# Kernel tuning notes

Measured on AMD Instinct MI355X. Metric: run time of the kernel, lower is better.

The kernel has to match this reference:

```python
import jax, jax.numpy as jnp
import numpy as np

BLOCK = 32  # mxfp8 block size along K


def setup_inputs() -> dict:
    key = jax.random.key(0)
    ks = jax.random.split(key, 7)
    TOK, IN, OUT, RANK = 8192, 4096, 4096, 64
    return {
        "input": jax.random.normal(ks[0], (TOK, IN), dtype=jnp.float32),
        "weight_q": jax.random.normal(ks[1], (OUT, IN), dtype=jnp.float32),
        "block_scale": jax.random.uniform(ks[2], (OUT, IN // BLOCK), dtype=jnp.float32),
        "bias": jax.random.normal(ks[3], (OUT,), dtype=jnp.float32),
        "svd_u": jax.random.normal(ks[4], (OUT, RANK), dtype=jnp.float32),
        "svd_s": jax.random.uniform(ks[5], (RANK,), dtype=jnp.float32),
        "svd_v": jax.random.normal(ks[6], (IN, RANK), dtype=jnp.float32),
    }


def _dequant_mxfp8(weight_q, block_scale):
    # weight_q: [M, K], block_scale: [M, K//BLOCK] -> per-block scaled weight [M, K]
    M, K = weight_q.shape
    nb = K // BLOCK
    w = weight_q.reshape(M, nb, BLOCK) * block_scale.reshape(M, nb, 1)
    return w.reshape(M, K)


def reference(input, weight_q, block_scale, bias, svd_u, svd_s, svd_v):
    # SVD outlier branch: ((input @ V) * S) @ U^T
    outlier = ((input @ svd_v) * svd_s[None, :]) @ svd_u.T  # [TOK, OUT]
    # Dequantize mxfp8 weight then linear: input @ W^T + bias
    w = _dequant_mxfp8(weight_q, block_scale)
    residual = input @ w.T + bias[None, :]
    return outlier + residual
```

## Files before the change

### kernel.cpp

```cpp
#include <hip/hip_runtime.h>
#include <stdint.h>

typedef unsigned short ushort_t;
typedef __attribute__((ext_vector_type(8))) short short8;
typedef __attribute__((ext_vector_type(8))) unsigned short ushort8;
typedef __attribute__((ext_vector_type(4))) float f32x4;

#define TOK 8192
#define DIM_IN 4096
#define DIM_OUT 4096
#define RANK 64
#define NT (DIM_IN / 64)

__device__ __forceinline__ ushort_t f2bf(float f) {
    unsigned u = __float_as_uint(f);
    unsigned r = (u + 0x7fffu + ((u >> 16) & 1u)) >> 16;
    return (ushort_t)r;
}

__device__ __forceinline__ void gload16(const void* g, void* l) {
    __builtin_amdgcn_global_load_lds(
        (const __attribute__((address_space(1))) unsigned int*)g,
        (__attribute__((address_space(3))) unsigned int*)l,
        16, 0, 0);
}

__global__ __launch_bounds__(256) void prep_input_k(const float* __restrict__ in,
                                                    ushort_t* __restrict__ out) {
    size_t idx = (size_t)blockIdx.x * 256 + threadIdx.x;
    const float4* p = (const float4*)(in + idx * 8);
    float4 f0 = p[0], f1 = p[1];
    ushort8 o;
    o[0] = f2bf(f0.x); o[1] = f2bf(f0.y); o[2] = f2bf(f0.z); o[3] = f2bf(f0.w);
    o[4] = f2bf(f1.x); o[5] = f2bf(f1.y); o[6] = f2bf(f1.z); o[7] = f2bf(f1.w);
    *(ushort8*)(out + idx * 8) = o;
}

__global__ __launch_bounds__(256) void prep_weight_k(const float* __restrict__ wq,
                                                     const float* __restrict__ scale,
                                                     const float* __restrict__ U,
                                                     const float* __restrict__ s,
                                                     const float* __restrict__ V,
                                                     ushort_t* __restrict__ Wb) {
    __shared__ float Us[128][64];
    __shared__ float Vs[128][64];
    int tid = threadIdx.x;
    int ob = blockIdx.x >> 5;
    int kb = blockIdx.x & 31;

#pragma unroll
    for (int j = 0; j < 8; ++j) {
        int c = j * 256 + tid;
        int row = c >> 4;
        int col = (c & 15) * 4;
        float4 u = *(const float4*)&U[(size_t)(ob * 128 + row) * RANK + col];
        float4 sv = *(const float4*)&s[col];
        u.x *= sv.x; u.y *= sv.y; u.z *= sv.z; u.w *= sv.w;
        *(float4*)&Us[row][col] = u;
        float4 v = *(const float4*)&V[(size_t)(kb * 128 + row) * RANK + col];
        *(float4*)&Vs[row][col] = v;
    }
    __syncthreads();

    int ty = tid >> 4, tx = tid & 15;
    float acc[8][8];
#pragma unroll
    for (int i = 0; i < 8; ++i)
#pragma unroll
        for (int j = 0; j < 8; ++j) acc[i][j] = 0.f;

#pragma unroll 4
    for (int r4 = 0; r4 < 16; ++r4) {
        float4 u[8], v[8];
#pragma unroll
        for (int i = 0; i < 8; ++i) u[i] = *(const float4*)&Us[ty * 8 + i][r4 * 4];
#pragma unroll
        for (int j = 0; j < 8; ++j) v[j] = *(const float4*)&Vs[tx * 8 + j][r4 * 4];
#pragma unroll
        for (int i = 0; i < 8; ++i)
#pragma unroll
            for (int j = 0; j < 8; ++j)
                acc[i][j] += u[i].x * v[j].x + u[i].y * v[j].y + u[i].z * v[j].z + u[i].w * v[j].w;
    }

#pragma unroll
    for (int i = 0; i < 8; ++i) {
        int o = ob * 128 + ty * 8 + i;
        int k0 = kb * 128 + tx * 8;
        float sc = scale[(size_t)o * (DIM_IN / 32) + (k0 >> 5)];
        float4 q0 = *(const float4*)&wq[(size_t)o * DIM_IN + k0];
        float4 q1 = *(const float4*)&wq[(size_t)o * DIM_IN + k0 + 4];
        ushort8 w;
        w[0] = f2bf(q0.x * sc + acc[i][0]);
        w[1] = f2bf(q0.y * sc + acc[i][1]);
        w[2] = f2bf(q0.z * sc + acc[i][2]);
        w[3] = f2bf(q0.w * sc + acc[i][3]);
        w[4] = f2bf(q1.x * sc + acc[i][4]);
        w[5] = f2bf(q1.y * sc + acc[i][5]);
        w[6] = f2bf(q1.z * sc + acc[i][6]);
        w[7] = f2bf(q1.w * sc + acc[i][7]);
        *(ushort8*)&Wb[(size_t)o * DIM_IN + k0] = w;
    }
}

__global__ __launch_bounds__(512, 2) void gemm_k(const ushort_t* __restrict__ A,
                                                 const ushort_t* __restrict__ B,
                                                 const float* __restrict__ bias,
                                                 float* __restrict__ C) {
    __shared__ ushort_t lds[2][2][2][8192];

    const int tid = threadIdx.x;
    const int wid = tid >> 6;
    const int lane = tid & 63;

    int bid = blockIdx.x;
    int swz = (bid & 7) * 64 + (bid >> 3);
    const int bm = swz >> 4;
    const int bn = swz & 15;

    const int wr = wid >> 2;
    const int wc = wid & 3;

    const int lane2 = lane ^ (((lane >> 5) & 1) << 1);
    const int srow = (wid >> 1) * 16 + (lane2 >> 2);
    const int scol = (wid & 1) * 32 + (lane2 & 3) * 8;
    const ushort_t* pa = A + (size_t)(bm * 256 + srow) * DIM_IN + scol;
    const ushort_t* pb = B + (size_t)(bn * 256 + srow) * DIM_IN + scol;

    const int loff = ((((lane & 15) * 64 + (lane >> 4) * 16) ^ (((lane >> 3) & 1) << 5)) >> 1);

    f32x4 acc[8][4] = {};

    auto stageA = [&](int buf, int half, int t) {
        const ushort_t* g = pa + (size_t)half * 128 * DIM_IN + t * 64;
        gload16(g, &lds[buf][0][half][wid * 512]);
        gload16(g + (size_t)64 * DIM_IN, &lds[buf][0][half][(wid + 8) * 512]);
    };
    auto stageB = [&](int buf, int half, int t) {
        const ushort_t* g = pb + (size_t)half * 128 * DIM_IN + t * 64;
        gload16(g, &lds[buf][1][half][wid * 512]);
        gload16(g + (size_t)64 * DIM_IN, &lds[buf][1][half][(wid + 8) * 512]);
    };

    auto tile_step = [&](int buf, int t, int mode) {
        const ushort_t* LA = &lds[buf][0][wr][0];
        const ushort_t* LB = &lds[buf][1][wc >> 1][0];
        const int bsub = (wc & 1) * 4;
        short8 aA[4], aB[4], bA[2][2], bB[2][2];

        auto rdA = [&](short8 (&dst)[4], int mhalf, int kk) {
#pragma unroll
            for (int m = 0; m < 4; ++m)
                dst[m] = *(const short8*)(LA + ((((mhalf * 4 + m) * 2) + kk) << 9) + loff);
        };
        auto rdB = [&](short8 (&dst)[2][2], int noff, int kk) {
#pragma unroll
            for (int n = 0; n < 2; ++n)
                dst[n][kk] = *(const short8*)(LB + ((((bsub + noff + n) * 2) + kk) << 9) + loff);
        };
        auto cluster = [&](short8 (&av)[4], short8 (&bv)[2][2], int kk, int mb, int nb) {
            __builtin_amdgcn_s_setprio(1);
#pragma unroll
            for (int m = 0; m < 4; ++m)
#pragma unroll
                for (int n = 0; n < 2; ++n)
                    acc[mb + m][nb + n] =
                        __builtin_amdgcn_mfma_f32_16x16x32_bf16(av[m], bv[n][kk], acc[mb + m][nb + n], 0, 0, 0);
            __builtin_amdgcn_s_setprio(0);
        };

        rdA(aA, 0, 0);
        rdB(bA, 0, 0);
        rdA(aB, 0, 1);
        rdB(bA, 0, 1);
        if (mode >= 1) stageA(buf ^ 1, 1, t + 1);
        cluster(aA, bA, 0, 0, 0);
        rdB(bB, 2, 0);
        cluster(aB, bA, 1, 0, 0);

        rdB(bB, 2, 1);
        cluster(aA, bB, 0, 0, 2);
        rdA(aA, 1, 0);
        cluster(aB, bB, 1, 0, 2);
        __builtin_amdgcn_s_barrier();

        rdA(aB, 1, 1);
        if (mode == 2) { stageB(buf, 0, t + 2); stageB(buf, 1, t + 2); }
        cluster(aA, bB, 0, 4, 2);
        cluster(aB, bB, 1, 4, 2);
        __builtin_amdgcn_s_barrier();

        if (mode == 2) stageA(buf, 0, t + 2);
        cluster(aA, bA, 0, 4, 0);
        cluster(aB, bA, 1, 4, 0);
        if (mode == 2)
            asm volatile("s_waitcnt vmcnt(6)" ::: "memory");
        else if (mode == 1)
            asm volatile("s_waitcnt vmcnt(0)" ::: "memory");
        if (mode >= 1) __builtin_amdgcn_s_barrier();
    };

    stageA(0, 0, 0); stageA(0, 1, 0); stageB(0, 0, 0); stageB(0, 1, 0);
    stageB(1, 0, 1); stageB(1, 1, 1); stageA(1, 0, 1);
    asm volatile("s_waitcnt vmcnt(6)" ::: "memory");
    __builtin_amdgcn_s_barrier();

    for (int t = 0; t < NT - 2; t += 2) {
        tile_step(0, t, 2);
        tile_step(1, t + 1, 2);
    }
    tile_step(0, NT - 2, 1);
    tile_step(1, NT - 1, 0);

    const int ccol = lane & 15;
    const int crow = (lane >> 4) * 4;
#pragma unroll
    for (int n = 0; n < 4; ++n) {
        int gcol = bn * 256 + wc * 64 + n * 16 + ccol;
        float bv = bias[gcol];
#pragma unroll
        for (int m = 0; m < 8; ++m) {
            size_t grow = (size_t)(bm * 256 + wr * 128 + m * 16 + crow);
#pragma unroll
            for (int r = 0; r < 4; ++r)
                C[(grow + r) * DIM_OUT + gcol] = acc[m][n][r] + bv;
        }
    }
}

extern "C" void kernel_launch(void* const* d_in, const int* in_sizes, int n_in,
                              void* d_out, int out_size, void* d_ws, size_t ws_size,
                              hipStream_t stream) {
    const float* input = (const float*)d_in[0];
    const float* wq    = (const float*)d_in[1];
    const float* scale = (const float*)d_in[2];
    const float* bias  = (const float*)d_in[3];
    const float* U     = (const float*)d_in[4];
    const float* s     = (const float*)d_in[5];
    const float* V     = (const float*)d_in[6];
    float* out = (float*)d_out;

    ushort_t* Abf = (ushort_t*)d_ws;
    ushort_t* Wbf = Abf + (size_t)TOK * DIM_IN;

    prep_input_k<<<(TOK * DIM_IN) / (256 * 8), 256, 0, stream>>>(input, Abf);
    prep_weight_k<<<(DIM_OUT / 128) * (DIM_IN / 128), 256, 0, stream>>>(wq, scale, U, s, V, Wbf);
    gemm_k<<<(TOK / 256) * (DIM_OUT / 256), 512, 0, stream>>>(Abf, Wbf, bias, out);
}
```

Before: 329.9 us.

## Compute low-rank U·S·V^T weight correction with bf16 MFMA in prep kernel

The weight-prep kernel, which folds the SVD outlier term into the dequantized weight, now computes the 128x128 U*S*V^T tile with bf16 MFMA instructions instead of scalar FP32 FMAs. U and V are converted to bf16 and written to XOR-swizzled LDS, and the MFMA result is staged back through padded LDS so the original per-thread output mapping still works. This removes the scalar FMA cost of the rank-64 product. In exchange, the low-rank correction is computed and stored in bf16 instead of FP32, which adds rounding error.

```diff
diff --git a/kernel.cpp b/kernel.cpp
--- a/kernel.cpp
+++ b/kernel.cpp
@@ -3,6 +3,7 @@
 
 typedef unsigned short ushort_t;
 typedef __attribute__((ext_vector_type(8))) short short8;
+typedef __attribute__((ext_vector_type(4))) unsigned short ushort4_t;
 typedef __attribute__((ext_vector_type(8))) unsigned short ushort8;
 typedef __attribute__((ext_vector_type(4))) float f32x4;
 
@@ -16,6 +17,9 @@
     unsigned u = __float_as_uint(f);
     unsigned r = (u + 0x7fffu + ((u >> 16) & 1u)) >> 16;
     return (ushort_t)r;
+}
+__device__ __forceinline__ float bf2f(ushort_t u) {
+    return __uint_as_float(((unsigned)u) << 16);
 }
 
 __device__ __forceinline__ void gload16(const void* g, void* l) {
@@ -42,63 +46,89 @@
                                                      const float* __restrict__ s,
                                                      const float* __restrict__ V,
                                                      ushort_t* __restrict__ Wb) {
-    __shared__ float Us[128][64];
-    __shared__ float Vs[128][64];
-    int tid = threadIdx.x;
-    int ob = blockIdx.x >> 5;
-    int kb = blockIdx.x & 31;
-
+    __shared__ ushort_t sm[18432];
+    const int tid = threadIdx.x;
+    const int wv = tid >> 6;
+    const int lane = tid & 63;
+    const int ob = blockIdx.x >> 5;
+    const int kb = blockIdx.x & 31;
+
+    char* smb = (char*)sm;
 #pragma unroll
     for (int j = 0; j < 8; ++j) {
-        int c = j * 256 + tid;
-        int row = c >> 4;
-        int col = (c & 15) * 4;
-        float4 u = *(const float4*)&U[(size_t)(ob * 128 + row) * RANK + col];
-        float4 sv = *(const float4*)&s[col];
-        u.x *= sv.x; u.y *= sv.y; u.z *= sv.z; u.w *= sv.w;
-        *(float4*)&Us[row][col] = u;
-        float4 v = *(const float4*)&V[(size_t)(kb * 128 + row) * RANK + col];
-        *(float4*)&Vs[row][col] = v;
+        int idx = j * 256 + tid;
+        int row = idx >> 4;
+        int c4 = idx & 15;
+        float4 sv = *(const float4*)&s[c4 * 4];
+        float4 u = *(const float4*)&U[(size_t)(ob * 128 + row) * RANK + c4 * 4];
+        ushort4_t up;
+        up[0] = f2bf(u.x * sv.x); up[1] = f2bf(u.y * sv.y);
+        up[2] = f2bf(u.z * sv.z); up[3] = f2bf(u.w * sv.w);
+        int wbyte = row * 128 + ((c4 * 8) ^ ((row & 7) << 4));
+        *(ushort4_t*)(smb + wbyte) = up;
+        float4 v = *(const float4*)&V[(size_t)(kb * 128 + row) * RANK + c4 * 4];
+        ushort4_t vp;
+        vp[0] = f2bf(v.x); vp[1] = f2bf(v.y); vp[2] = f2bf(v.z); vp[3] = f2bf(v.w);
+        *(ushort4_t*)(smb + 16384 + wbyte) = vp;
     }
     __syncthreads();
 
-    int ty = tid >> 4, tx = tid & 15;
-    float acc[8][8];
-#pragma unroll
-    for (int i = 0; i < 8; ++i)
-#pragma unroll
-        for (int j = 0; j < 8; ++j) acc[i][j] = 0.f;
-
-#pragma unroll 4
-    for (int r4 = 0; r4 < 16; ++r4) {
-        float4 u[8], v[8];
-#pragma unroll
-        for (int i = 0; i < 8; ++i) u[i] = *(const float4*)&Us[ty * 8 + i][r4 * 4];
-#pragma unroll
-        for (int j = 0; j < 8; ++j) v[j] = *(const float4*)&Vs[tx * 8 + j][r4 * 4];
-#pragma unroll
-        for (int i = 0; i < 8; ++i)
-#pragma unroll
-            for (int j = 0; j < 8; ++j)
-                acc[i][j] += u[i].x * v[j].x + u[i].y * v[j].y + u[i].z * v[j].z + u[i].w * v[j].w;
-    }
-
+    const int wr = wv >> 1, wc = wv & 1;
+    f32x4 acc[4][4] = {};
+    {
+        short8 a[4], b[4];
+#pragma unroll
+        for (int kk = 0; kk < 2; ++kk) {
+#pragma unroll
+            for (int f = 0; f < 4; ++f) {
+                int r = wr * 64 + f * 16 + (lane & 15);
+                int kbyte = ((lane >> 4) * 16 + kk * 64) ^ ((r & 7) << 4);
+                a[f] = *(const short8*)(smb + r * 128 + kbyte);
+                int r2 = wc * 64 + f * 16 + (lane & 15);
+                int kbyte2 = ((lane >> 4) * 16 + kk * 64) ^ ((r2 & 7) << 4);
+                b[f] = *(const short8*)(smb + 16384 + r2 * 128 + kbyte2);
+            }
+#pragma unroll
+            for (int fm = 0; fm < 4; ++fm)
+#pragma unroll
+                for (int fn = 0; fn < 4; ++fn)
+                    acc[fm][fn] = __builtin_amdgcn_mfma_f32_16x16x32_bf16(
+                        a[fm], b[fn], acc[fm][fn], 0, 0, 0);
+        }
+    }
+    __syncthreads();
+
+#pragma unroll
+    for (int fm = 0; fm < 4; ++fm)
+#pragma unroll
+        for (int fn = 0; fn < 4; ++fn) {
+            int row0 = wr * 64 + fm * 16 + (lane >> 4) * 4;
+            int col = wc * 64 + fn * 16 + (lane & 15);
+#pragma unroll
+            for (int r = 0; r < 4; ++r)
+                sm[(row0 + r) * 136 + col] = f2bf(acc[fm][fn][r]);
+        }
+    __syncthreads();
+
+    const int ty = tid >> 4, tx = tid & 15;
 #pragma unroll
     for (int i = 0; i < 8; ++i) {
-        int o = ob * 128 + ty * 8 + i;
+        int ol = ty * 8 + i;
+        int o = ob * 128 + ol;
         int k0 = kb * 128 + tx * 8;
         float sc = scale[(size_t)o * (DIM_IN / 32) + (k0 >> 5)];
         float4 q0 = *(const float4*)&wq[(size_t)o * DIM_IN + k0];
         float4 q1 = *(const float4*)&wq[(size_t)o * DIM_IN + k0 + 4];
+        ushort8 sv8 = *(const ushort8*)&sm[ol * 136 + tx * 8];
         ushort8 w;
-        w[0] = f2bf(q0.x * sc + acc[i][0]);
-        w[1] = f2bf(q0.y * sc + acc[i][1]);
-        w[2] = f2bf(q0.z * sc + acc[i][2]);
-        w[3] = f2bf(q0.w * sc + acc[i][3]);
-        w[4] = f2bf(q1.x * sc + acc[i][4]);
-        w[5] = f2bf(q1.y * sc + acc[i][5]);
-        w[6] = f2bf(q1.z * sc + acc[i][6]);
-        w[7] = f2bf(q1.w * sc + acc[i][7]);
+        w[0] = f2bf(q0.x * sc + bf2f(sv8[0]));
+        w[1] = f2bf(q0.y * sc + bf2f(sv8[1]));
+        w[2] = f2bf(q0.z * sc + bf2f(sv8[2]));
+        w[3] = f2bf(q0.w * sc + bf2f(sv8[3]));
+        w[4] = f2bf(q1.x * sc + bf2f(sv8[4]));
+        w[5] = f2bf(q1.y * sc + bf2f(sv8[5]));
+        w[6] = f2bf(q1.z * sc + bf2f(sv8[6]));
+        w[7] = f2bf(q1.w * sc + bf2f(sv8[7]));
         *(ushort8*)&Wb[(size_t)o * DIM_IN + k0] = w;
     }
 }
```

New measurement: 286.7 us (median of 2 runs). 1.15x faster.
